# Performance work log

Hardware: AMD Instinct MI355X
Metric: run time of the kernel (lower is better)

## Reference

```python
import jax, jax.numpy as jnp
import numpy as np

MAX_IT = 20
LAMBDA_ROF = 7.0
SIGMA = 1.0 / (7.0 * 0.01)
TAU = 0.01
THETA = 0.5

H, W_DIM = 4096, 4096


def forward_weighted_gradient(x, w):
    # x: (1,H,W), w: (2,H,W) -> (2,H,W)
    x0 = x[0]
    gh = jnp.pad(x0[:, 1:] - x0[:, :-1], ((0, 0), (0, 1)))   # grad[0,:, :-1]
    gv = jnp.pad(x0[1:, :] - x0[:-1, :], ((0, 1), (0, 0)))   # grad[1,:-1,:]
    return jnp.stack([gh, gv], axis=0) * w


def backward_divergence(y):
    # y: (2,H,W) -> (1,H,W)
    yh, yv = y[0], y[1]
    d_h = jnp.concatenate(
        [yh[:, :1], yh[:, 1:-1] - yh[:, :-2], -yh[:, -2:-1]], axis=1)
    d_v = jnp.concatenate(
        [yv[:1, :], yv[1:-1, :] - yv[:-2, :], -yv[-2:-1, :]], axis=0)
    return (d_h + d_v)[None]


def prox_linf_ball(p, r):
    # p - detach(max(p-r,0) - max(-p-r,0))  (clamp treated as data in torch code)
    shrink = jnp.maximum(p - r, 0.0) - jnp.maximum(-p - r, 0.0)
    return p - jax.lax.stop_gradient(shrink)


def setup_inputs() -> dict:
    key = jax.random.key(0)
    k1, _ = jax.random.split(key)
    img_obs = jax.random.uniform(k1, (1, H, W_DIM), dtype=jnp.float32)
    w = jnp.ones((2, H, W_DIM), dtype=jnp.float32)
    return {"img_obs": img_obs, "w": w}


def reference(img_obs, w):
    x0 = img_obs
    x_tilde0 = img_obs
    y0 = jnp.zeros((2,) + img_obs.shape[1:], dtype=img_obs.dtype)

    def step(carry, _):
        x, x_tilde, y = carry
        y = y + SIGMA * forward_weighted_gradient(x_tilde, w)
        y = prox_linf_ball(y, 1.0)
        x_old = x
        x = (x + TAU * backward_divergence(y)
             + LAMBDA_ROF * TAU * img_obs) / (1.0 + LAMBDA_ROF * TAU)
        x_tilde = x + THETA * (x - x_old)
        return (x, x_tilde, y), None

    (x, x_tilde, y), _ = jax.lax.scan(step, (x0, x_tilde0, y0), None, length=MAX_IT)
    return x_tilde
```

## Files before the change

kernel.cpp:

```cpp
#include <hip/hip_runtime.h>

static constexpr int H = 4096;
static constexpr int W = 4096;
static constexpr long N = (long)H * W;

static constexpr int TILE = 64;
static constexpr int HOFF = 12;
static constexpr int R    = TILE + 2*HOFF;
static constexpr int S    = R;
static constexpr int PS   = R * S;
static constexpr int CPR  = R / 8;
static constexpr int NCH  = R * CPR;
static constexpr int NT   = 512;

static constexpr float SIGMA = 14.285714285714286f;
static constexpr float INVD  = 1.0f / 1.07f;
static constexpr float TIV   = 0.01f / 1.07f;
static constexpr float CF    = 0.07f / 1.07f;

typedef _Float16 half8  __attribute__((ext_vector_type(8)));
typedef _Float16 half4v __attribute__((ext_vector_type(4)));

__device__ __forceinline__ half8 splat8(float f) {
    _Float16 h = (_Float16)f;
    half8 v = {h, h, h, h, h, h, h, h};
    return v;
}
__device__ __forceinline__ half8 clamp8(half8 v) {
    v = __builtin_elementwise_min(v, splat8(1.0f));
    v = __builtin_elementwise_max(v, splat8(-1.0f));
    return v;
}

__global__ __launch_bounds__(256) void pack_w(
    const float* __restrict__ wg, _Float16* __restrict__ whp, _Float16* __restrict__ wvp)
{
    const long p = ((long)blockIdx.x * 256 + threadIdx.x) * 8;
    const int i = (int)(p >> 12);
    const float4* hp = reinterpret_cast<const float4*>(wg + p);
    float4 a = hp[0], b = hp[1];
    const float4* vp = reinterpret_cast<const float4*>(wg + N + p);
    float4 c = vp[0], d = vp[1];
    half8 wh, wv;
    wh[0]=(_Float16)(SIGMA*a.x); wh[1]=(_Float16)(SIGMA*a.y);
    wh[2]=(_Float16)(SIGMA*a.z); wh[3]=(_Float16)(SIGMA*a.w);
    wh[4]=(_Float16)(SIGMA*b.x); wh[5]=(_Float16)(SIGMA*b.y);
    wh[6]=(_Float16)(SIGMA*b.z); wh[7]=(_Float16)(SIGMA*b.w);
    wv[0]=(_Float16)(SIGMA*c.x); wv[1]=(_Float16)(SIGMA*c.y);
    wv[2]=(_Float16)(SIGMA*c.z); wv[3]=(_Float16)(SIGMA*c.w);
    wv[4]=(_Float16)(SIGMA*d.x); wv[5]=(_Float16)(SIGMA*d.y);
    wv[6]=(_Float16)(SIGMA*d.z); wv[7]=(_Float16)(SIGMA*d.w);
    if ((p & 4095) + 8 == W) wh[7] = (_Float16)0.0f;
    if (i == H - 1) wv = splat8(0.0f);
    *reinterpret_cast<half8*>(whp + p) = wh;
    *reinterpret_cast<half8*>(wvp + p) = wv;
}

template<int PHASE>
__global__ __launch_bounds__(NT, 4) void fused_pd(
    const float* __restrict__ img,
    const _Float16* __restrict__ whp, const _Float16* __restrict__ wvp,
    _Float16* __restrict__ xg,  _Float16* __restrict__ xtg,
    _Float16* __restrict__ yhg, _Float16* __restrict__ yvg,
    float* __restrict__ out)
{
    __shared__ _Float16 lds_s[2 * PS + NCH + 2];
    _Float16* __restrict__ xtp = lds_s;
    _Float16* __restrict__ yvp = lds_s + PS;
    _Float16* __restrict__ yhe = lds_s + 2 * PS;

    const int tid = threadIdx.x;
    const int gi0 = blockIdx.y * TILE - HOFF;
    const int gj0 = blockIdx.x * TILE - HOFF;
    const bool interior = (gi0 >= 0) && (gj0 >= 0) && (gi0 + R <= H) && (gj0 + R <= W);

    const int t0 = tid, t1 = tid + NT;
    const int i0_ = t0 / CPR, i1_ = t1 / CPR;
    const int b0 = i0_ * S + (t0 - i0_ * CPR) * 8;
    const int b1 = i1_ * S + (t1 - i1_ * CPR) * 8;
    const bool act1 = (t1 < NCH);

    const half8 kTIV  = splat8(TIV);
    const half8 kINVD = splat8(INVD);
    const half8 k15   = splat8(1.5f);
    const half8 kM05  = splat8(-0.5f);

    half8 wh0, wh1, wv0, wv1;
    half8 ci0, ci1;
    half8 x0, x1;
    half8 xt0r, xt1r;
    half8 yh0, yh1, yv0, yv1;

    auto loadC = [&](int t, half8& whr, half8& wvr, half8& cir, half8& xr,
                     half8& xtr, half8& yhr, half8& yvr) {
        const int i  = t / CPR;
        const int j0 = (t - i * CPR) * 8;
        const int gi = gi0 + i;
        const int gj = gj0 + j0;
        if (interior) {
            const long o = (long)gi * W + gj;
            const float4* ip = reinterpret_cast<const float4*>(img + o);
            float4 a = ip[0], b = ip[1];
            float im[8] = {a.x, a.y, a.z, a.w, b.x, b.y, b.z, b.w};
            whr = *reinterpret_cast<const half8*>(whp + o);
            wvr = *reinterpret_cast<const half8*>(wvp + o);
#pragma unroll
            for (int k = 0; k < 8; ++k) cir[k] = (_Float16)(CF * im[k]);
            if (PHASE == 0) {
#pragma unroll
                for (int k = 0; k < 8; ++k) xr[k] = (_Float16)im[k];
                xtr = xr;
                yhr = splat8(0.f); yvr = splat8(0.f);
            } else {
                xr  = *reinterpret_cast<const half8*>(xg  + o);
                xtr = *reinterpret_cast<const half8*>(xtg + o);
                yhr = *reinterpret_cast<const half8*>(yhg + o);
                yvr = *reinterpret_cast<const half8*>(yvg + o);
            }
        } else {
            const int gic = min(max(gi, 0), H - 1);
            const bool rowin = (gi >= 0) && (gi < H);
#pragma unroll
            for (int k = 0; k < 8; ++k) {
                const int gjk = gj + k;
                const int gjc = min(max(gjk, 0), W - 1);
                const bool inim = rowin && (gjk >= 0) && (gjk < W);
                const long o = (long)gic * W + gjc;
                const float imf = img[o];
                whr[k] = inim ? whp[o] : (_Float16)0.0f;
                wvr[k] = inim ? wvp[o] : (_Float16)0.0f;
                cir[k] = (_Float16)(CF * imf);
                if (PHASE == 0) {
                    xr[k]  = (_Float16)imf;
                    xtr[k] = (_Float16)imf;
                    yhr[k] = (_Float16)0.0f;
                    yvr[k] = (_Float16)0.0f;
                } else {
                    xr[k]  = xg[o];
                    xtr[k] = xtg[o];
                    yhr[k] = inim ? yhg[o] : (_Float16)0.0f;
                    yvr[k] = inim ? yvg[o] : (_Float16)0.0f;
                }
            }
        }
        *reinterpret_cast<half8*>(xtp + i * S + j0) = xtr;
    };
    loadC(t0, wh0, wv0, ci0, x0, xt0r, yh0, yv0);
    if (act1) loadC(t1, wh1, wv1, ci1, x1, xt1r, yh1, yv1);
    if (tid == 0) yhe[0] = (_Float16)0.0f;
    __syncthreads();

    for (int it = 0; it < 10; ++it) {
        auto dualC = [&](int t, int base, half8 cv, half8 wh, half8 wv,
                         half8& yh, half8& yv) {
            _Float16 rt = xtp[base + 8];
            half8 bv = *reinterpret_cast<const half8*>(xtp + base + S);
            half8 sh = __builtin_shufflevector(cv, cv, 1, 2, 3, 4, 5, 6, 7, 7);
            sh[7] = rt;
            yh = clamp8((sh - cv) * wh + yh);
            yv = clamp8((bv - cv) * wv + yv);
            *reinterpret_cast<half8*>(yvp + base) = yv;
            yhe[t + 1] = yh[7];
        };
        dualC(t0, b0, xt0r, wh0, wv0, yh0, yv0);
        if (act1) dualC(t1, b1, xt1r, wh1, wv1, yh1, yv1);
        __syncthreads();

        auto primC = [&](int t, int base, half8 yh, half8 yv, half8 ci,
                         half8& x, half8& xtr) {
            _Float16 yl = yhe[t];
            half8 yva = *reinterpret_cast<const half8*>(yvp + base - S);
            half8 ysh = __builtin_shufflevector(yh, yh, 0, 0, 1, 2, 3, 4, 5, 6);
            ysh[0] = yl;
            half8 dv = (yh - ysh) + (yv - yva);
            half8 tt = dv * kTIV + ci;
            half8 xn = x * kINVD + tt;
            half8 xt = xn * k15 + x * kM05;
            x = xn;
            xtr = xt;
            *reinterpret_cast<half8*>(xtp + base) = xt;
        };
        primC(t0, b0, yh0, yv0, ci0, x0, xt0r);
        if (act1) primC(t1, b1, yh1, yv1, ci1, x1, xt1r);
        __syncthreads();
    }

    const int r  = tid >> 3;
    const int k  = tid & 7;
    const int lb = (HOFF + r) * S + HOFF + k * 8;
    const long gb = (long)(blockIdx.y * TILE + r) * W + blockIdx.x * TILE + k * 8;

    if (PHASE == 0) {
        {
            half4v a0 = *reinterpret_cast<const half4v*>(xtp + lb);
            half4v a1 = *reinterpret_cast<const half4v*>(xtp + lb + 4);
            half8 o; o[0]=a0[0];o[1]=a0[1];o[2]=a0[2];o[3]=a0[3];
                     o[4]=a1[0];o[5]=a1[1];o[6]=a1[2];o[7]=a1[3];
            *reinterpret_cast<half8*>(xtg + gb) = o;
            half4v b0v = *reinterpret_cast<const half4v*>(yvp + lb);
            half4v b1v = *reinterpret_cast<const half4v*>(yvp + lb + 4);
            half8 o2; o2[0]=b0v[0];o2[1]=b0v[1];o2[2]=b0v[2];o2[3]=b0v[3];
                      o2[4]=b1v[0];o2[5]=b1v[1];o2[6]=b1v[2];o2[7]=b1v[3];
            *reinterpret_cast<half8*>(yvg + gb) = o2;
        }
        __syncthreads();
        *reinterpret_cast<half8*>(xtp + b0) = x0;
        *reinterpret_cast<half8*>(yvp + b0) = yh0;
        if (act1) {
            *reinterpret_cast<half8*>(xtp + b1) = x1;
            *reinterpret_cast<half8*>(yvp + b1) = yh1;
        }
        __syncthreads();
        {
            half4v a0 = *reinterpret_cast<const half4v*>(xtp + lb);
            half4v a1 = *reinterpret_cast<const half4v*>(xtp + lb + 4);
            half8 o; o[0]=a0[0];o[1]=a0[1];o[2]=a0[2];o[3]=a0[3];
                     o[4]=a1[0];o[5]=a1[1];o[6]=a1[2];o[7]=a1[3];
            *reinterpret_cast<half8*>(xg + gb) = o;
            half4v b0v = *reinterpret_cast<const half4v*>(yvp + lb);
            half4v b1v = *reinterpret_cast<const half4v*>(yvp + lb + 4);
            half8 o2; o2[0]=b0v[0];o2[1]=b0v[1];o2[2]=b0v[2];o2[3]=b0v[3];
                      o2[4]=b1v[0];o2[5]=b1v[1];o2[6]=b1v[2];o2[7]=b1v[3];
            *reinterpret_cast<half8*>(yhg + gb) = o2;
        }
    } else {
        half4v a = *reinterpret_cast<const half4v*>(xtp + lb);
        half4v b = *reinterpret_cast<const half4v*>(xtp + lb + 4);
        float4 o0 = make_float4((float)a[0], (float)a[1], (float)a[2], (float)a[3]);
        float4 o1 = make_float4((float)b[0], (float)b[1], (float)b[2], (float)b[3]);
        *reinterpret_cast<float4*>(out + gb)     = o0;
        *reinterpret_cast<float4*>(out + gb + 4) = o1;
    }
}

extern "C" void kernel_launch(void* const* d_in, const int* in_sizes, int n_in,
                              void* d_out, int out_size, void* d_ws, size_t ws_size,
                              hipStream_t stream) {
    const float* img = (const float*)d_in[0];
    const float* wg  = (const float*)d_in[1];
    float* out = (float*)d_out;

    _Float16* ws16 = (_Float16*)d_ws;
    _Float16* whp = ws16;
    _Float16* wvp = ws16 + N;
    _Float16* xg  = ws16 + 2 * N;
    _Float16* xtg = ws16 + 3 * N;
    _Float16* yhg = ws16 + 4 * N;
    _Float16* yvg = ws16 + 5 * N;

    pack_w<<<dim3((int)(N / 8 / 256)), dim3(256), 0, stream>>>(wg, whp, wvp);

    dim3 grid(W / TILE, H / TILE);
    fused_pd<0><<<grid, dim3(NT), 0, stream>>>(img, whp, wvp, xg, xtg, yhg, yvg, out);
    fused_pd<1><<<grid, dim3(NT), 0, stream>>>(img, whp, wvp, xg, xtg, yhg, yvg, out);
}
```

Baseline: 369.4 us.

## Shift phase split to after dual update to drop x_tilde global buffer

Phase 0 now runs one extra dual update after its ten iterations and stores the updated dual instead of x_tilde. Phase 1 starts with a primal step using the loaded dual values and runs nine full iterations. This removes the x_tilde workspace array and its global write and read, cutting traffic between the two launches. The cost is reshuffled iteration bookkeeping and an extra LDS staging of yv and yhe during the phase 1 load.

Measured after the change: 344.6 us. 1.07x faster.

```diff
diff --git a/kernel.cpp b/kernel.cpp
--- a/kernel.cpp
+++ b/kernel.cpp
@@ -60,8 +60,7 @@
 __global__ __launch_bounds__(NT, 4) void fused_pd(
     const float* __restrict__ img,
     const _Float16* __restrict__ whp, const _Float16* __restrict__ wvp,
-    _Float16* __restrict__ xg,  _Float16* __restrict__ xtg,
-    _Float16* __restrict__ yhg, _Float16* __restrict__ yvg,
+    _Float16* __restrict__ xg, _Float16* __restrict__ yhg, _Float16* __restrict__ yvg,
     float* __restrict__ out)
 {
     __shared__ _Float16 lds_s[2 * PS + NCH + 2];
@@ -113,7 +112,6 @@
                 yhr = splat8(0.f); yvr = splat8(0.f);
             } else {
                 xr  = *reinterpret_cast<const half8*>(xg  + o);
-                xtr = *reinterpret_cast<const half8*>(xtg + o);
                 yhr = *reinterpret_cast<const half8*>(yhg + o);
                 yvr = *reinterpret_cast<const half8*>(yvg + o);
             }
@@ -137,51 +135,93 @@
                     yvr[k] = (_Float16)0.0f;
                 } else {
                     xr[k]  = xg[o];
-                    xtr[k] = xtg[o];
                     yhr[k] = inim ? yhg[o] : (_Float16)0.0f;
                     yvr[k] = inim ? yvg[o] : (_Float16)0.0f;
                 }
             }
         }
-        *reinterpret_cast<half8*>(xtp + i * S + j0) = xtr;
+        const int base = i * S + j0;
+        if (PHASE == 0) {
+            *reinterpret_cast<half8*>(xtp + base) = xtr;
+        } else {
+            *reinterpret_cast<half8*>(xtp + base) = xr;
+            *reinterpret_cast<half8*>(yvp + base) = yvr;
+            yhe[t + 1] = yhr[7];
+        }
     };
     loadC(t0, wh0, wv0, ci0, x0, xt0r, yh0, yv0);
     if (act1) loadC(t1, wh1, wv1, ci1, x1, xt1r, yh1, yv1);
     if (tid == 0) yhe[0] = (_Float16)0.0f;
     __syncthreads();
 
-    for (int it = 0; it < 10; ++it) {
-        auto dualC = [&](int t, int base, half8 cv, half8 wh, half8 wv,
-                         half8& yh, half8& yv) {
-            _Float16 rt = xtp[base + 8];
-            half8 bv = *reinterpret_cast<const half8*>(xtp + base + S);
-            half8 sh = __builtin_shufflevector(cv, cv, 1, 2, 3, 4, 5, 6, 7, 7);
-            sh[7] = rt;
-            yh = clamp8((sh - cv) * wh + yh);
-            yv = clamp8((bv - cv) * wv + yv);
-            *reinterpret_cast<half8*>(yvp + base) = yv;
-            yhe[t + 1] = yh[7];
-        };
-        dualC(t0, b0, xt0r, wh0, wv0, yh0, yv0);
-        if (act1) dualC(t1, b1, xt1r, wh1, wv1, yh1, yv1);
-        __syncthreads();
-
-        auto primC = [&](int t, int base, half8 yh, half8 yv, half8 ci,
-                         half8& x, half8& xtr) {
-            _Float16 yl = yhe[t];
-            half8 yva = *reinterpret_cast<const half8*>(yvp + base - S);
-            half8 ysh = __builtin_shufflevector(yh, yh, 0, 0, 1, 2, 3, 4, 5, 6);
-            ysh[0] = yl;
-            half8 dv = (yh - ysh) + (yv - yva);
-            half8 tt = dv * kTIV + ci;
-            half8 xn = x * kINVD + tt;
-            half8 xt = xn * k15 + x * kM05;
-            x = xn;
-            xtr = xt;
-            *reinterpret_cast<half8*>(xtp + base) = xt;
-        };
-        primC(t0, b0, yh0, yv0, ci0, x0, xt0r);
-        if (act1) primC(t1, b1, yh1, yv1, ci1, x1, xt1r);
+    auto dual_all = [&](bool write_yhe) {
+        _Float16 rt0 = xtp[b0 + 8];
+        half8 bv0 = *reinterpret_cast<const half8*>(xtp + b0 + S);
+        _Float16 rt1 = (_Float16)0.f; half8 bv1;
+        if (act1) {
+            rt1 = xtp[b1 + 8];
+            bv1 = *reinterpret_cast<const half8*>(xtp + b1 + S);
+        }
+        {
+            half8 sh = __builtin_shufflevector(xt0r, xt0r, 1, 2, 3, 4, 5, 6, 7, 7);
+            sh[7] = rt0;
+            yh0 = clamp8((sh - xt0r) * wh0 + yh0);
+            yv0 = clamp8((bv0 - xt0r) * wv0 + yv0);
+            *reinterpret_cast<half8*>(yvp + b0) = yv0;
+            if (write_yhe) yhe[t0 + 1] = yh0[7];
+        }
+        if (act1) {
+            half8 sh = __builtin_shufflevector(xt1r, xt1r, 1, 2, 3, 4, 5, 6, 7, 7);
+            sh[7] = rt1;
+            yh1 = clamp8((sh - xt1r) * wh1 + yh1);
+            yv1 = clamp8((bv1 - xt1r) * wv1 + yv1);
+            *reinterpret_cast<half8*>(yvp + b1) = yv1;
+            if (write_yhe) yhe[t1 + 1] = yh1[7];
+        }
+    };
+    auto prim_all = [&]() {
+        _Float16 yl0 = yhe[t0];
+        half8 yva0 = *reinterpret_cast<const half8*>(yvp + b0 - S);
+        _Float16 yl1 = (_Float16)0.f; half8 yva1;
+        if (act1) {
+            yl1  = yhe[t1];
+            yva1 = *reinterpret_cast<const half8*>(yvp + b1 - S);
+        }
+        {
+            half8 ysh = __builtin_shufflevector(yh0, yh0, 0, 0, 1, 2, 3, 4, 5, 6);
+            ysh[0] = yl0;
+            half8 dv = (yh0 - ysh) + (yv0 - yva0);
+            half8 tt = dv * kTIV + ci0;
+            half8 xn = x0 * kINVD + tt;
+            half8 xt = xn * k15 + x0 * kM05;
+            x0 = xn; xt0r = xt;
+            *reinterpret_cast<half8*>(xtp + b0) = xt;
+        }
+        if (act1) {
+            half8 ysh = __builtin_shufflevector(yh1, yh1, 0, 0, 1, 2, 3, 4, 5, 6);
+            ysh[0] = yl1;
+            half8 dv = (yh1 - ysh) + (yv1 - yva1);
+            half8 tt = dv * kTIV + ci1;
+            half8 xn = x1 * kINVD + tt;
+            half8 xt = xn * k15 + x1 * kM05;
+            x1 = xn; xt1r = xt;
+            *reinterpret_cast<half8*>(xtp + b1) = xt;
+        }
+    };
+
+    if (PHASE == 1) {
+        prim_all();
+        __syncthreads();
+    }
+    const int NIT = (PHASE == 0) ? 10 : 9;
+    for (int it = 0; it < NIT; ++it) {
+        dual_all(true);
+        __syncthreads();
+        prim_all();
+        __syncthreads();
+    }
+    if (PHASE == 0) {
+        dual_all(false);
         __syncthreads();
     }
 
@@ -192,16 +232,11 @@
 
     if (PHASE == 0) {
         {
-            half4v a0 = *reinterpret_cast<const half4v*>(xtp + lb);
-            half4v a1 = *reinterpret_cast<const half4v*>(xtp + lb + 4);
+            half4v a0 = *reinterpret_cast<const half4v*>(yvp + lb);
+            half4v a1 = *reinterpret_cast<const half4v*>(yvp + lb + 4);
             half8 o; o[0]=a0[0];o[1]=a0[1];o[2]=a0[2];o[3]=a0[3];
                      o[4]=a1[0];o[5]=a1[1];o[6]=a1[2];o[7]=a1[3];
-            *reinterpret_cast<half8*>(xtg + gb) = o;
-            half4v b0v = *reinterpret_cast<const half4v*>(yvp + lb);
-            half4v b1v = *reinterpret_cast<const half4v*>(yvp + lb + 4);
-            half8 o2; o2[0]=b0v[0];o2[1]=b0v[1];o2[2]=b0v[2];o2[3]=b0v[3];
-                      o2[4]=b1v[0];o2[5]=b1v[1];o2[6]=b1v[2];o2[7]=b1v[3];
-            *reinterpret_cast<half8*>(yvg + gb) = o2;
+            *reinterpret_cast<half8*>(yvg + gb) = o;
         }
         __syncthreads();
         *reinterpret_cast<half8*>(xtp + b0) = x0;
@@ -244,13 +279,12 @@
     _Float16* whp = ws16;
     _Float16* wvp = ws16 + N;
     _Float16* xg  = ws16 + 2 * N;
-    _Float16* xtg = ws16 + 3 * N;
-    _Float16* yhg = ws16 + 4 * N;
-    _Float16* yvg = ws16 + 5 * N;
+    _Float16* yhg = ws16 + 3 * N;
+    _Float16* yvg = ws16 + 4 * N;
 
     pack_w<<<dim3((int)(N / 8 / 256)), dim3(256), 0, stream>>>(wg, whp, wvp);
 
     dim3 grid(W / TILE, H / TILE);
-    fused_pd<0><<<grid, dim3(NT), 0, stream>>>(img, whp, wvp, xg, xtg, yhg, yvg, out);
-    fused_pd<1><<<grid, dim3(NT), 0, stream>>>(img, whp, wvp, xg, xtg, yhg, yvg, out);
-}
+    fused_pd<0><<<grid, dim3(NT), 0, stream>>>(img, whp, wvp, xg, yhg, yvg, out);
+    fused_pd<1><<<grid, dim3(NT), 0, stream>>>(img, whp, wvp, xg, yhg, yvg, out);
+}
```
